# Performance work log

Hardware: AMD Instinct MI355X
Metric: run time of the kernel (lower is better)

## Reference

```python
import jax, jax.numpy as jnp
import numpy as np

# dims
B, T = 64, 512
L = 3                 # number of HMLSTM layers
IN = 512              # per-layer input size (all equal)
D = L * IN            # 1536 total input size
E = 1024              # embedding_size
H1, H2 = 1024, 1024   # linear_sizes
O = 512               # output_size


def setup_inputs() -> dict:
    key = jax.random.key(0)
    ks = jax.random.split(key, 12)
    s = 0.02
    return {
        "x": jax.random.normal(ks[0], (B, T, D), dtype=jnp.float32),
        # gate linears: Linear(sum(input_sizes) -> 1, bias=False), one per layer, stacked [L, D]
        "Wg": jax.random.normal(ks[1], (L, D), dtype=jnp.float32) * s,
        # per-layer embedding linears Linear(IN -> E), stacked [L, E, IN] / [L, E]
        "We": jax.random.normal(ks[2], (L, E, IN), dtype=jnp.float32) * s,
        "be": jax.random.normal(ks[3], (L, E), dtype=jnp.float32) * s,
        # tanh MLP stack
        "W1": jax.random.normal(ks[4], (H1, E), dtype=jnp.float32) * s,
        "b1": jax.random.normal(ks[5], (H1,), dtype=jnp.float32) * s,
        "W2": jax.random.normal(ks[6], (H2, H1), dtype=jnp.float32) * s,
        "b2": jax.random.normal(ks[7], (H2,), dtype=jnp.float32) * s,
        # output head
        "Wo": jax.random.normal(ks[8], (O, H2), dtype=jnp.float32) * s,
        "bo": jax.random.normal(ks[9], (O,), dtype=jnp.float32) * s,
    }


def reference(x, Wg, We, be, W1, b1, W2, b2, Wo, bo):
    b, t, d = x.shape
    h = x.reshape(b * t, d)                       # per-timestep features, fully batched over time
    # gates: sigmoid(Linear(full h -> 1)) per layer -> [N, L]
    g = jax.nn.sigmoid(h @ Wg.T)
    # split full input into per-layer chunks (equal sizes -> reshape) and gate them
    hl = h.reshape(b * t, L, IN) * g[:, :, None]  # [N, L, IN]
    # s = sum_l Linear_l(h_l * g_l); biases sum since each embedding adds its own bias
    s = jnp.einsum("nli,lei->ne", hl, We) + be.sum(axis=0)
    he = jax.nn.relu(s)
    # fnn: tanh-activated linear stack
    o = jnp.tanh(he @ W1.T + b1)
    o = jnp.tanh(o @ W2.T + b2)
    out = o @ Wo.T + bo
    return out.reshape(b, t, O)
```

## Files before the change

kernel.cpp:

```cpp
#include <hip/hip_runtime.h>
#include <math.h>


typedef __attribute__((ext_vector_type(8))) short short8;
typedef __attribute__((ext_vector_type(4))) float float4v;

#define DEV __device__ __forceinline__

DEV unsigned short f2bf(float f){
    union{float f; unsigned int i;} c; c.f = f;
    unsigned int r = c.i + 0x7fffu + ((c.i>>16)&1u);
    return (unsigned short)(r>>16);
}
DEV unsigned int pack2(float a, float b){
    return (unsigned int)f2bf(a) | ((unsigned int)f2bf(b)<<16);
}

DEV void gload_lds16(const unsigned short* g, unsigned short* l){
    __builtin_amdgcn_global_load_lds((const __attribute__((address_space(1))) void*)g,
                                     (__attribute__((address_space(3))) void*)l, 16, 0, 0);
}

__global__ __launch_bounds__(256) void cvt_flat(const float* __restrict__ src,
                                                unsigned short* __restrict__ dst, int n8)
{
    int v = blockIdx.x*256 + threadIdx.x;
    if(v >= n8) return;
    const float4* s = (const float4*)(src) + v*2;
    float4 a = s[0], b = s[1];
    uint4 o;
    o.x = pack2(a.x, a.y); o.y = pack2(a.z, a.w);
    o.z = pack2(b.x, b.y); o.w = pack2(b.z, b.w);
    *((uint4*)dst + v) = o;
}

__global__ __launch_bounds__(256) void cvt_we(const float* __restrict__ We,
                                              unsigned short* __restrict__ Wep)
{
    int v  = blockIdx.x*256 + threadIdx.x;
    int i8 = v & 63;
    int e  = (v>>6) & 1023;
    int l  = v>>16;
    const float4* s = (const float4*)(We + (size_t)l*524288 + (size_t)e*512 + i8*8);
    float4 a = s[0], b = s[1];
    uint4 o;
    o.x = pack2(a.x, a.y); o.y = pack2(a.z, a.w);
    o.z = pack2(b.x, b.y); o.w = pack2(b.z, b.w);
    *(uint4*)(Wep + (size_t)e*1536 + (size_t)l*512 + i8*8) = o;
}

__global__ __launch_bounds__(256) void gate_u(const float* __restrict__ x,
                                              const float* __restrict__ Wg,
                                              unsigned short* __restrict__ u)
{
    int row  = blockIdx.x*4 + (threadIdx.x>>6);
    int lane = threadIdx.x & 63;
    const float4* xr = (const float4*)(x + (size_t)row*1536);
    float4 hv[6];
    #pragma unroll
    for(int j=0;j<6;j++) hv[j] = xr[j*64 + lane];

    float p[3];
    #pragma unroll
    for(int l=0;l<3;l++){
        const float4* wr = (const float4*)(Wg + (size_t)l*1536);
        float s = 0.f;
        #pragma unroll
        for(int j=0;j<6;j++){
            float4 wv = wr[j*64 + lane];
            s += hv[j].x*wv.x + hv[j].y*wv.y + hv[j].z*wv.z + hv[j].w*wv.w;
        }
        p[l] = s;
    }
    #pragma unroll
    for(int off=32; off; off>>=1){
        p[0] += __shfl_xor(p[0], off);
        p[1] += __shfl_xor(p[1], off);
        p[2] += __shfl_xor(p[2], off);
    }
    float g[3];
    #pragma unroll
    for(int l=0;l<3;l++) g[l] = 1.f/(1.f + __expf(-p[l]));

    uint2* ur = (uint2*)(u + (size_t)row*1536);
    #pragma unroll
    for(int j=0;j<6;j++){
        float gj = g[(j*64+lane)>>7];
        uint2 o;
        o.x = pack2(hv[j].x*gj, hv[j].y*gj);
        o.y = pack2(hv[j].z*gj, hv[j].w*gj);
        ur[j*64 + lane] = o;
    }
}

template<int ACT, int BIAS_ROWS, bool F32OUT>
__global__ __launch_bounds__(512, 2) void gemm256(
    const unsigned short* __restrict__ A,
    const unsigned short* __restrict__ W,
    const float* __restrict__ bias,
    void* __restrict__ Cv,
    int M, int N, int K)
{
    __shared__ __align__(128) unsigned short As[2*2*128*64];
    __shared__ __align__(128) unsigned short Bs[2*2*128*64];

    const int tid = threadIdx.x;
    const int nb  = N >> 8;
    const int mt  = M >> 8;
    const int xcd = blockIdx.x & 7;
    const int j   = blockIdx.x >> 3;
    const int bm  = xcd*(mt>>3) + j/nb;
    const int bn  = j % nb;
    const int m0  = bm << 8, n0 = bn << 8;

    const int lane = tid & 63, wid = tid >> 6;
    const int wm = wid >> 2, wn = wid & 3;
    const int lr = lane & 15, quad = lane >> 4, sx = lr & 7;
    const int srow = lane >> 3;
    const int scb  = (lane & 7) ^ srow;
    const size_t aoff = (size_t)srow*K + scb*8;
    const int nt = K >> 6;

    float4v acc[8][4];
    #pragma unroll
    for(int i=0;i<8;i++)
        #pragma unroll
        for(int jj=0;jj<4;jj++) acc[i][jj] = (float4v){0.f,0.f,0.f,0.f};

#define STAGE_A(h,l,s) gload_lds16(A + ((size_t)(m0 + (h)*128 + (l)*64 + wid*8))*K + (s)*64 + aoff, \
                                   &As[(((s)&1)*2+(h))*8192 + ((l)*64 + wid*8)*64])
#define STAGE_B(h,l,s) gload_lds16(W + ((size_t)(n0 + (h)*128 + (l)*64 + wid*8))*K + (s)*64 + aoff, \
                                   &Bs[(((s)&1)*2+(h))*8192 + ((l)*64 + wid*8)*64])

    STAGE_A(0,0,0); STAGE_A(0,1,0); STAGE_A(1,0,0); STAGE_A(1,1,0);
    STAGE_B(0,0,0); STAGE_B(0,1,0); STAGE_B(1,0,0); STAGE_B(1,1,0);
    if(nt > 1){
        STAGE_B(0,0,1); STAGE_B(0,1,1); STAGE_B(1,0,1); STAGE_B(1,1,1);
        STAGE_A(0,0,1); STAGE_A(1,0,1);
        asm volatile("s_waitcnt vmcnt(6)" ::: "memory");
    } else {
        asm volatile("s_waitcnt vmcnt(0)" ::: "memory");
    }
    __builtin_amdgcn_s_barrier();

    for(int t=0; t<nt; ++t){
        const int cur = t & 1;
        const unsigned short* Ab = &As[(cur*2 + wm)*8192];
        const unsigned short* Bb = &Bs[(cur*2 + (wn>>1))*8192 + (wn&1)*4096];
        short8 bfr[4][2];
        #pragma unroll
        for(int q=0; q<4; ++q){
            short8 af[2][2];
            #pragma unroll
            for(int mi=0; mi<2; ++mi)
                #pragma unroll
                for(int ks=0; ks<2; ++ks)
                    af[mi][ks] = *(const short8*)&Ab[(q*32 + mi*16 + lr)*64 + (((ks*4+quad)^sx)*8)];
            if(q==0){
                #pragma unroll
                for(int ni=0; ni<4; ++ni)
                    #pragma unroll
                    for(int ks=0; ks<2; ++ks)
                        bfr[ni][ks] = *(const short8*)&Bb[(ni*16 + lr)*64 + (((ks*4+quad)^sx)*8)];
            }
            if(q==0)      { if(t+1 < nt){ STAGE_A(0,1,t+1); STAGE_A(1,1,t+1); } }
            else if(q==1) { if(t+2 < nt){ STAGE_B(0,0,t+2); STAGE_B(0,1,t+2); } }
            else if(q==2) { if(t+2 < nt){ STAGE_B(1,0,t+2); STAGE_B(1,1,t+2); } }
            else          { if(t+2 < nt){ STAGE_A(0,0,t+2); STAGE_A(1,0,t+2); } }
            __builtin_amdgcn_s_barrier();
            __builtin_amdgcn_s_setprio(1);
            #pragma unroll
            for(int ks=0; ks<2; ++ks)
                #pragma unroll
                for(int mi=0; mi<2; ++mi)
                    #pragma unroll
                    for(int ni=0; ni<4; ++ni)
                        acc[q*2+mi][ni] = __builtin_amdgcn_mfma_f32_16x16x32_bf16(
                            af[mi][ks], bfr[ni][ks], acc[q*2+mi][ni], 0, 0, 0);
            __builtin_amdgcn_s_setprio(0);
            if(q < 3) __builtin_amdgcn_s_barrier();
        }
        if(t+2 < nt) asm volatile("s_waitcnt vmcnt(6)" ::: "memory");
        else         asm volatile("s_waitcnt vmcnt(0)" ::: "memory");
        __builtin_amdgcn_s_barrier();
    }
#undef STAGE_A
#undef STAGE_B

    #pragma unroll
    for(int ni=0; ni<4; ++ni){
        const int n = n0 + wn*64 + ni*16 + lr;
        float bsum = 0.f;
        #pragma unroll
        for(int r=0; r<BIAS_ROWS; ++r) bsum += bias[(size_t)r*N + n];
        #pragma unroll
        for(int Q=0; Q<8; ++Q){
            #pragma unroll
            for(int reg=0; reg<4; ++reg){
                const int m = m0 + wm*128 + Q*16 + quad*4 + reg;
                float v = acc[Q][ni][reg] + bsum;
                if(ACT==1)      v = fmaxf(v, 0.f);
                else if(ACT==2) v = tanhf(v);
                if constexpr (F32OUT) ((float*)Cv)[(size_t)m*N + n] = v;
                else                  ((unsigned short*)Cv)[(size_t)m*N + n] = f2bf(v);
            }
        }
    }
}

extern "C" void kernel_launch(void* const* d_in, const int* in_sizes, int n_in,
                              void* d_out, int out_size, void* d_ws, size_t ws_size,
                              hipStream_t stream)
{
    const float* x  = (const float*)d_in[0];
    const float* Wg = (const float*)d_in[1];
    const float* We = (const float*)d_in[2];
    const float* be = (const float*)d_in[3];
    const float* W1 = (const float*)d_in[4];
    const float* b1 = (const float*)d_in[5];
    const float* W2 = (const float*)d_in[6];
    const float* b2 = (const float*)d_in[7];
    const float* Wo = (const float*)d_in[8];
    const float* bo = (const float*)d_in[9];
    float* out = (float*)d_out;

    const int M = 32768;

    char* w = (char*)d_ws;
    unsigned short* Wep   = (unsigned short*)w; w += (size_t)1024*1536*2;
    unsigned short* W1b   = (unsigned short*)w; w += (size_t)1024*1024*2;
    unsigned short* W2b   = (unsigned short*)w; w += (size_t)1024*1024*2;
    unsigned short* Wob   = (unsigned short*)w; w += (size_t)512*1024*2;
    unsigned short* slotA = (unsigned short*)w; w += (size_t)M*1536*2;
    unsigned short* slotB = (unsigned short*)w; w += (size_t)M*1024*2;
    unsigned short* u  = slotA;
    unsigned short* o1 = slotA;
    unsigned short* he = slotB;
    unsigned short* o2 = slotB;

    hipLaunchKernelGGL(cvt_flat, dim3(512), dim3(256), 0, stream, W1, W1b, 131072);
    hipLaunchKernelGGL(cvt_flat, dim3(512), dim3(256), 0, stream, W2, W2b, 131072);
    hipLaunchKernelGGL(cvt_flat, dim3(256), dim3(256), 0, stream, Wo, Wob, 65536);
    hipLaunchKernelGGL(cvt_we,   dim3(768), dim3(256), 0, stream, We, Wep);

    hipLaunchKernelGGL(gate_u, dim3(M/4), dim3(256), 0, stream, x, Wg, u);
    hipLaunchKernelGGL((gemm256<1,3,false>), dim3((M/256)*(1024/256)), dim3(512), 0, stream,
                       u,  Wep, be, he,  M, 1024, 1536);
    hipLaunchKernelGGL((gemm256<2,1,false>), dim3((M/256)*(1024/256)), dim3(512), 0, stream,
                       he, W1b, b1, o1,  M, 1024, 1024);
    hipLaunchKernelGGL((gemm256<2,1,false>), dim3((M/256)*(1024/256)), dim3(512), 0, stream,
                       o1, W2b, b2, o2,  M, 1024, 1024);
    hipLaunchKernelGGL((gemm256<0,1,true>),  dim3((M/256)*(512/256)),  dim3(512), 0, stream,
                       o2, Wob, bo, out, M, 512, 1024);
}
```

Before: 684.3 us.

## Merge prep kernels into one launch and unroll GEMM K-loop by two buffers

The four weight-conversion kernels and the gate kernel are merged into a single launch that dispatches on block index, which removes four launch gaps. The GEMM main loop is unrolled by two, so the LDS double-buffer index becomes a compile-time constant. Explicit lgkmcnt waits are added around the barrier so the B-fragment LDS reads overlap with issuing the async global-to-LDS copies. The loop now assumes the K-tile count is even and at least two, which holds for the K values used here.

```diff
diff --git a/kernel.cpp b/kernel.cpp
--- a/kernel.cpp
+++ b/kernel.cpp
@@ -21,76 +21,82 @@
                                      (__attribute__((address_space(3))) void*)l, 16, 0, 0);
 }
 
-__global__ __launch_bounds__(256) void cvt_flat(const float* __restrict__ src,
-                                                unsigned short* __restrict__ dst, int n8)
+__global__ __launch_bounds__(256) void prep(
+    const float* __restrict__ x,  const float* __restrict__ Wg,
+    const float* __restrict__ W1, const float* __restrict__ W2,
+    const float* __restrict__ Wo, const float* __restrict__ We,
+    unsigned short* __restrict__ u,   unsigned short* __restrict__ W1b,
+    unsigned short* __restrict__ W2b, unsigned short* __restrict__ Wob,
+    unsigned short* __restrict__ Wep)
 {
-    int v = blockIdx.x*256 + threadIdx.x;
-    if(v >= n8) return;
-    const float4* s = (const float4*)(src) + v*2;
-    float4 a = s[0], b = s[1];
-    uint4 o;
-    o.x = pack2(a.x, a.y); o.y = pack2(a.z, a.w);
-    o.z = pack2(b.x, b.y); o.w = pack2(b.z, b.w);
-    *((uint4*)dst + v) = o;
-}
-
-__global__ __launch_bounds__(256) void cvt_we(const float* __restrict__ We,
-                                              unsigned short* __restrict__ Wep)
-{
-    int v  = blockIdx.x*256 + threadIdx.x;
+    int b = blockIdx.x;
+    if(b < 8192){
+        int row  = b*4 + (threadIdx.x>>6);
+        int lane = threadIdx.x & 63;
+        const float4* xr = (const float4*)(x + (size_t)row*1536);
+        float4 hv[6];
+        #pragma unroll
+        for(int j=0;j<6;j++) hv[j] = xr[j*64 + lane];
+
+        float p[3];
+        #pragma unroll
+        for(int l=0;l<3;l++){
+            const float4* wr = (const float4*)(Wg + (size_t)l*1536);
+            float s = 0.f;
+            #pragma unroll
+            for(int j=0;j<6;j++){
+                float4 wv = wr[j*64 + lane];
+                s += hv[j].x*wv.x + hv[j].y*wv.y + hv[j].z*wv.z + hv[j].w*wv.w;
+            }
+            p[l] = s;
+        }
+        #pragma unroll
+        for(int off=32; off; off>>=1){
+            p[0] += __shfl_xor(p[0], off);
+            p[1] += __shfl_xor(p[1], off);
+            p[2] += __shfl_xor(p[2], off);
+        }
+        float g[3];
+        #pragma unroll
+        for(int l=0;l<3;l++) g[l] = 1.f/(1.f + __expf(-p[l]));
+
+        uint2* ur = (uint2*)(u + (size_t)row*1536);
+        #pragma unroll
+        for(int j=0;j<6;j++){
+            float gj = g[(j*64+lane)>>7];
+            uint2 o;
+            o.x = pack2(hv[j].x*gj, hv[j].y*gj);
+            o.y = pack2(hv[j].z*gj, hv[j].w*gj);
+            ur[j*64 + lane] = o;
+        }
+        return;
+    }
+    b -= 8192;
+    if(b < 1280){
+        const float* src; unsigned short* dst; int v0;
+        if(b < 512)      { src = W1; dst = W1b; v0 = b<<8; }
+        else if(b < 1024){ src = W2; dst = W2b; v0 = (b-512)<<8; }
+        else             { src = Wo; dst = Wob; v0 = (b-1024)<<8; }
+        int v = v0 + threadIdx.x;
+        const float4* s = (const float4*)(src) + (size_t)v*2;
+        float4 a = s[0], c = s[1];
+        uint4 o;
+        o.x = pack2(a.x, a.y); o.y = pack2(a.z, a.w);
+        o.z = pack2(c.x, c.y); o.w = pack2(c.z, c.w);
+        *((uint4*)dst + v) = o;
+        return;
+    }
+    b -= 1280;
+    int v  = b*256 + threadIdx.x;
     int i8 = v & 63;
     int e  = (v>>6) & 1023;
     int l  = v>>16;
     const float4* s = (const float4*)(We + (size_t)l*524288 + (size_t)e*512 + i8*8);
-    float4 a = s[0], b = s[1];
+    float4 a = s[0], c = s[1];
     uint4 o;
     o.x = pack2(a.x, a.y); o.y = pack2(a.z, a.w);
-    o.z = pack2(b.x, b.y); o.w = pack2(b.z, b.w);
+    o.z = pack2(c.x, c.y); o.w = pack2(c.z, c.w);
     *(uint4*)(Wep + (size_t)e*1536 + (size_t)l*512 + i8*8) = o;
-}
-
-__global__ __launch_bounds__(256) void gate_u(const float* __restrict__ x,
-                                              const float* __restrict__ Wg,
-                                              unsigned short* __restrict__ u)
-{
-    int row  = blockIdx.x*4 + (threadIdx.x>>6);
-    int lane = threadIdx.x & 63;
-    const float4* xr = (const float4*)(x + (size_t)row*1536);
-    float4 hv[6];
-    #pragma unroll
-    for(int j=0;j<6;j++) hv[j] = xr[j*64 + lane];
-
-    float p[3];
-    #pragma unroll
-    for(int l=0;l<3;l++){
-        const float4* wr = (const float4*)(Wg + (size_t)l*1536);
-        float s = 0.f;
-        #pragma unroll
-        for(int j=0;j<6;j++){
-            float4 wv = wr[j*64 + lane];
-            s += hv[j].x*wv.x + hv[j].y*wv.y + hv[j].z*wv.z + hv[j].w*wv.w;
-        }
-        p[l] = s;
-    }
-    #pragma unroll
-    for(int off=32; off; off>>=1){
-        p[0] += __shfl_xor(p[0], off);
-        p[1] += __shfl_xor(p[1], off);
-        p[2] += __shfl_xor(p[2], off);
-    }
-    float g[3];
-    #pragma unroll
-    for(int l=0;l<3;l++) g[l] = 1.f/(1.f + __expf(-p[l]));
-
-    uint2* ur = (uint2*)(u + (size_t)row*1536);
-    #pragma unroll
-    for(int j=0;j<6;j++){
-        float gj = g[(j*64+lane)>>7];
-        uint2 o;
-        o.x = pack2(hv[j].x*gj, hv[j].y*gj);
-        o.y = pack2(hv[j].z*gj, hv[j].w*gj);
-        ur[j*64 + lane] = o;
-    }
 }
 
 template<int ACT, int BIAS_ROWS, bool F32OUT>
@@ -127,62 +133,63 @@
         #pragma unroll
         for(int jj=0;jj<4;jj++) acc[i][jj] = (float4v){0.f,0.f,0.f,0.f};
 
-#define STAGE_A(h,l,s) gload_lds16(A + ((size_t)(m0 + (h)*128 + (l)*64 + wid*8))*K + (s)*64 + aoff, \
-                                   &As[(((s)&1)*2+(h))*8192 + ((l)*64 + wid*8)*64])
-#define STAGE_B(h,l,s) gload_lds16(W + ((size_t)(n0 + (h)*128 + (l)*64 + wid*8))*K + (s)*64 + aoff, \
-                                   &Bs[(((s)&1)*2+(h))*8192 + ((l)*64 + wid*8)*64])
-
-    STAGE_A(0,0,0); STAGE_A(0,1,0); STAGE_A(1,0,0); STAGE_A(1,1,0);
-    STAGE_B(0,0,0); STAGE_B(0,1,0); STAGE_B(1,0,0); STAGE_B(1,1,0);
-    if(nt > 1){
-        STAGE_B(0,0,1); STAGE_B(0,1,1); STAGE_B(1,0,1); STAGE_B(1,1,1);
-        STAGE_A(0,0,1); STAGE_A(1,0,1);
-        asm volatile("s_waitcnt vmcnt(6)" ::: "memory");
-    } else {
-        asm volatile("s_waitcnt vmcnt(0)" ::: "memory");
-    }
+#define STAGE_A(h,l,s,P) gload_lds16(A + ((size_t)(m0 + (h)*128 + (l)*64 + wid*8))*K + (size_t)(s)*64 + aoff, \
+                                     &As[((P)*2+(h))*8192 + ((l)*64 + wid*8)*64])
+#define STAGE_B(h,l,s,P) gload_lds16(W + ((size_t)(n0 + (h)*128 + (l)*64 + wid*8))*K + (size_t)(s)*64 + aoff, \
+                                     &Bs[((P)*2+(h))*8192 + ((l)*64 + wid*8)*64])
+
+    STAGE_A(0,0,0,0); STAGE_A(0,1,0,0); STAGE_A(1,0,0,0); STAGE_A(1,1,0,0);
+    STAGE_B(0,0,0,0); STAGE_B(0,1,0,0); STAGE_B(1,0,0,0); STAGE_B(1,1,0,0);
+    STAGE_B(0,0,1,1); STAGE_B(0,1,1,1); STAGE_B(1,0,1,1); STAGE_B(1,1,1,1);
+    STAGE_A(0,0,1,1); STAGE_A(1,0,1,1);
+    asm volatile("s_waitcnt vmcnt(6)" ::: "memory");
     __builtin_amdgcn_s_barrier();
 
-    for(int t=0; t<nt; ++t){
-        const int cur = t & 1;
-        const unsigned short* Ab = &As[(cur*2 + wm)*8192];
-        const unsigned short* Bb = &Bs[(cur*2 + (wn>>1))*8192 + (wn&1)*4096];
-        short8 bfr[4][2];
-        #pragma unroll
-        for(int q=0; q<4; ++q){
-            short8 af[2][2];
+    for(int tt=0; tt<nt; tt+=2){
+        #pragma unroll
+        for(int uu=0; uu<2; ++uu){
+            const int T = tt + uu;
+            const unsigned short* Ab = &As[(uu*2 + wm)*8192];
+            const unsigned short* Bb = &Bs[(uu*2 + (wn>>1))*8192 + (wn&1)*4096];
+            short8 bfr[4][2];
             #pragma unroll
-            for(int mi=0; mi<2; ++mi)
-                #pragma unroll
-                for(int ks=0; ks<2; ++ks)
-                    af[mi][ks] = *(const short8*)&Ab[(q*32 + mi*16 + lr)*64 + (((ks*4+quad)^sx)*8)];
-            if(q==0){
-                #pragma unroll
-                for(int ni=0; ni<4; ++ni)
-                    #pragma unroll
-                    for(int ks=0; ks<2; ++ks)
-                        bfr[ni][ks] = *(const short8*)&Bb[(ni*16 + lr)*64 + (((ks*4+quad)^sx)*8)];
-            }
-            if(q==0)      { if(t+1 < nt){ STAGE_A(0,1,t+1); STAGE_A(1,1,t+1); } }
-            else if(q==1) { if(t+2 < nt){ STAGE_B(0,0,t+2); STAGE_B(0,1,t+2); } }
-            else if(q==2) { if(t+2 < nt){ STAGE_B(1,0,t+2); STAGE_B(1,1,t+2); } }
-            else          { if(t+2 < nt){ STAGE_A(0,0,t+2); STAGE_A(1,0,t+2); } }
-            __builtin_amdgcn_s_barrier();
-            __builtin_amdgcn_s_setprio(1);
-            #pragma unroll
-            for(int ks=0; ks<2; ++ks)
+            for(int q=0; q<4; ++q){
+                short8 af[2][2];
                 #pragma unroll
                 for(int mi=0; mi<2; ++mi)
                     #pragma unroll
+                    for(int ks=0; ks<2; ++ks)
+                        af[mi][ks] = *(const short8*)&Ab[(q*32 + mi*16 + lr)*64 + (((ks*4+quad)^sx)*8)];
+                if(q==0){
+                    #pragma unroll
                     for(int ni=0; ni<4; ++ni)
-                        acc[q*2+mi][ni] = __builtin_amdgcn_mfma_f32_16x16x32_bf16(
-                            af[mi][ks], bfr[ni][ks], acc[q*2+mi][ni], 0, 0, 0);
-            __builtin_amdgcn_s_setprio(0);
-            if(q < 3) __builtin_amdgcn_s_barrier();
-        }
-        if(t+2 < nt) asm volatile("s_waitcnt vmcnt(6)" ::: "memory");
-        else         asm volatile("s_waitcnt vmcnt(0)" ::: "memory");
-        __builtin_amdgcn_s_barrier();
+                        #pragma unroll
+                        for(int ks=0; ks<2; ++ks)
+                            bfr[ni][ks] = *(const short8*)&Bb[(ni*16 + lr)*64 + (((ks*4+quad)^sx)*8)];
+                }
+                if(q==0)      { if(T+1 < nt){ STAGE_A(0,1,T+1,1-uu); STAGE_A(1,1,T+1,1-uu); } }
+                else if(q==1) { if(T+2 < nt){ STAGE_B(0,0,T+2,uu);   STAGE_B(0,1,T+2,uu);   } }
+                else if(q==2) { if(T+2 < nt){ STAGE_B(1,0,T+2,uu);   STAGE_B(1,1,T+2,uu);   } }
+                else          { if(T+2 < nt){ STAGE_A(0,0,T+2,uu);   STAGE_A(1,0,T+2,uu);   } }
+                if(q==0) asm volatile("s_waitcnt lgkmcnt(8)");
+                __builtin_amdgcn_s_barrier();
+                asm volatile("s_waitcnt lgkmcnt(0)");
+                __builtin_amdgcn_s_setprio(1);
+                #pragma unroll
+                for(int ks=0; ks<2; ++ks)
+                    #pragma unroll
+                    for(int mi=0; mi<2; ++mi)
+                        #pragma unroll
+                        for(int ni=0; ni<4; ++ni)
+                            acc[q*2+mi][ni] = __builtin_amdgcn_mfma_f32_16x16x32_bf16(
+                                af[mi][ks], bfr[ni][ks], acc[q*2+mi][ni], 0, 0, 0);
+                __builtin_amdgcn_s_setprio(0);
+                if(q < 3) __builtin_amdgcn_s_barrier();
+            }
+            if(T+2 < nt) asm volatile("s_waitcnt vmcnt(6)" ::: "memory");
+            else         asm volatile("s_waitcnt vmcnt(0)" ::: "memory");
+            __builtin_amdgcn_s_barrier();
+        }
     }
 #undef STAGE_A
 #undef STAGE_B
@@ -238,12 +245,9 @@
     unsigned short* he = slotB;
     unsigned short* o2 = slotB;
 
-    hipLaunchKernelGGL(cvt_flat, dim3(512), dim3(256), 0, stream, W1, W1b, 131072);
-    hipLaunchKernelGGL(cvt_flat, dim3(512), dim3(256), 0, stream, W2, W2b, 131072);
-    hipLaunchKernelGGL(cvt_flat, dim3(256), dim3(256), 0, stream, Wo, Wob, 65536);
-    hipLaunchKernelGGL(cvt_we,   dim3(768), dim3(256), 0, stream, We, Wep);
-
-    hipLaunchKernelGGL(gate_u, dim3(M/4), dim3(256), 0, stream, x, Wg, u);
+    hipLaunchKernelGGL(prep, dim3(10240), dim3(256), 0, stream,
+                       x, Wg, W1, W2, Wo, We, u, W1b, W2b, Wob, Wep);
+
     hipLaunchKernelGGL((gemm256<1,3,false>), dim3((M/256)*(1024/256)), dim3(512), 0, stream,
                        u,  Wep, be, he,  M, 1024, 1536);
     hipLaunchKernelGGL((gemm256<2,1,false>), dim3((M/256)*(1024/256)), dim3(512), 0, stream,
```

Result: faster. 652.4 us (-4.7%).
